# Optimization experiments

Hardware: AMD Instinct MI355X
Metric: run time of the kernel (lower is better)

The kernel has to match this reference:

```python
import jax, jax.numpy as jnp
import numpy as np

K_NEIGHBORS = 16
IGNORE_INDEX = -1
LOSS_WEIGHT = 1.0
N_POINTS = 262144
NUM_CLASSES = 20


def setup_inputs() -> dict:
    key = jax.random.key(0)
    k1, k2, k3, k4 = jax.random.split(key, 4)
    seg_logits = jax.random.normal(k1, (N_POINTS, NUM_CLASSES), dtype=jnp.float32)
    coord = jax.random.normal(k2, (N_POINTS, 3), dtype=jnp.float32)
    labels = jax.random.randint(k3, (N_POINTS,), 0, NUM_CLASSES, dtype=jnp.int64)
    # KNN indices are computed under no_grad in the original (pointops.knn_query);
    # here they are synthetic in-range indices (no -1 padding entries).
    reference_index = jax.random.randint(k4, (N_POINTS, K_NEIGHBORS), 0, N_POINTS, dtype=jnp.int64)
    return {
        "seg_logits": seg_logits,
        "coord": coord,
        "labels": labels,
        "reference_index": reference_index,
    }


def reference(seg_logits, coord, labels, reference_index):
    # coord is only used by the (no-grad) KNN query in the original; indices are given.
    probs = jax.nn.softmax(seg_logits, axis=1)              # [N, C]
    idx = jnp.maximum(reference_index, 0)                   # safe gather index
    knn_mask = reference_index >= 0                         # sign(idx+1).bool()
    neighbor_labels = labels[idx]                           # [N, k]
    same_label_mask = labels[:, None] == neighbor_labels
    center_valid = (labels != IGNORE_INDEX)[:, None]
    neighbor_valid = neighbor_labels != IGNORE_INDEX
    total_mask = knn_mask & center_valid & neighbor_valid & same_label_mask  # [N, k]

    neighbor_probs = probs[idx]                             # [N, k, C]
    prob_dist_sq = jnp.sum((probs[:, None, :] - neighbor_probs) ** 2, axis=2)  # [N, k]
    sum_loss = jnp.sum(prob_dist_sq * total_mask.astype(probs.dtype))
    num_valid = jnp.maximum(jnp.sum(total_mask).astype(probs.dtype), 1.0)
    return (sum_loss / num_valid) * LOSS_WEIGHT
```

## Files before the change

### kernel.cpp

```cpp
#include <hip/hip_runtime.h>

#define NCLS 20
#define IGNORE_INDEX (-1)
#define TPB 128
#define PAIRS_PER_THREAD 8
#define PPB (TPB * PAIRS_PER_THREAD)
#define BLOCKS 4096
#define RBITS 18

__device__ __forceinline__ void softmax_row(const float* __restrict__ row, float* v) {
    const float4* r4 = (const float4*)row;
#pragma unroll
    for (int q = 0; q < 5; ++q) {
        float4 t = r4[q];
        v[4 * q + 0] = t.x; v[4 * q + 1] = t.y;
        v[4 * q + 2] = t.z; v[4 * q + 3] = t.w;
    }
    float mx = v[0];
#pragma unroll
    for (int c = 1; c < NCLS; ++c) mx = fmaxf(mx, v[c]);
    float s = 0.f;
#pragma unroll
    for (int c = 0; c < NCLS; ++c) { v[c] = __expf(v[c] - mx); s += v[c]; }
    float inv = 1.0f / s;
#pragma unroll
    for (int c = 0; c < NCLS; ++c) v[c] *= inv;
}

__global__ __launch_bounds__(TPB) void fused_kernel(
    const float* __restrict__ logits, const int* __restrict__ labels,
    const int* __restrict__ ref_idx,
    unsigned int* __restrict__ counts, float* __restrict__ partials,
    long long total_pairs) {
    __shared__ unsigned int s_buf[PPB];
    __shared__ int s_cnt;
    __shared__ float s_wsum[TPB / 64];
    const int tid = threadIdx.x;
    if (tid == 0) s_cnt = 0;
    __syncthreads();

    const long long pair0 = (long long)blockIdx.x * PPB + (long long)tid * 8;
    if (pair0 + 8 <= total_pairs) {
        const int p = (int)(pair0 >> 4);
        const int li = labels[p];
        int4 ra = *(const int4*)(ref_idx + pair0);
        int4 rb = *(const int4*)(ref_idx + pair0 + 4);
        int rr[8] = {ra.x, ra.y, ra.z, ra.w, rb.x, rb.y, rb.z, rb.w};
        int nl[8];
#pragma unroll
        for (int j = 0; j < 8; ++j) nl[j] = labels[max(rr[j], 0)];
        if (li != IGNORE_INDEX) {
#pragma unroll
            for (int j = 0; j < 8; ++j) {
                if (rr[j] >= 0 && nl[j] == li) {
                    int slot = atomicAdd(&s_cnt, 1);
                    s_buf[slot] = ((unsigned int)(tid * 8 + j) << RBITS) |
                                  (unsigned int)rr[j];
                }
            }
        }
    }
    __syncthreads();
    const int c = s_cnt;

    float fsum = 0.f;
    for (int i = tid; i < c; i += TPB) {
        unsigned int e = s_buf[i];
        unsigned int lid = e >> RBITS;
        unsigned int r = e & ((1u << RBITS) - 1u);
        unsigned int p = (unsigned int)blockIdx.x * (PPB / 16) + (lid >> 4);
        float a[NCLS], b[NCLS];
        softmax_row(logits + (size_t)p * NCLS, a);
        softmax_row(logits + (size_t)r * NCLS, b);
        float d = 0.f;
#pragma unroll
        for (int k = 0; k < NCLS; ++k) {
            float dx = a[k] - b[k];
            d = fmaf(dx, dx, d);
        }
        fsum += d;
    }

#pragma unroll
    for (int off = 32; off > 0; off >>= 1) fsum += __shfl_down(fsum, off, 64);
    if ((tid & 63) == 0) s_wsum[tid >> 6] = fsum;
    __syncthreads();
    if (tid == 0) {
        float t = 0.f;
#pragma unroll
        for (int w = 0; w < TPB / 64; ++w) t += s_wsum[w];
        partials[blockIdx.x] = t;
        counts[blockIdx.x] = (unsigned int)c;
    }
}

__global__ __launch_bounds__(1024) void reduce_kernel(
    const float* __restrict__ partials, const unsigned int* __restrict__ counts,
    float* __restrict__ out, int m) {
    double dsum = 0.0;
    unsigned long long cnt = 0;
    for (int i = threadIdx.x; i < m; i += 1024) {
        dsum += (double)partials[i];
        cnt  += (unsigned long long)min(counts[i], (unsigned int)PPB);
    }
#pragma unroll
    for (int off = 32; off > 0; off >>= 1) {
        dsum += __shfl_down(dsum, off, 64);
        cnt  += __shfl_down(cnt,  off, 64);
    }
    __shared__ double s_sum[16];
    __shared__ unsigned long long s_cnt[16];
    const int wave = threadIdx.x >> 6;
    if ((threadIdx.x & 63) == 0) { s_sum[wave] = dsum; s_cnt[wave] = cnt; }
    __syncthreads();
    if (threadIdx.x == 0) {
        double ts = 0.0; unsigned long long tc = 0;
        for (int w = 0; w < 16; ++w) { ts += s_sum[w]; tc += s_cnt[w]; }
        if (tc < 1ull) tc = 1ull;
        out[0] = (float)(ts / (double)tc);
    }
}

extern "C" void kernel_launch(void* const* d_in, const int* in_sizes, int n_in,
                              void* d_out, int out_size, void* d_ws, size_t ws_size,
                              hipStream_t stream) {
    const float* seg_logits = (const float*)d_in[0];
    const int* labels  = (const int*)d_in[2];
    const int* ref_idx = (const int*)d_in[3];
    float* out = (float*)d_out;
    const int n = in_sizes[2];
    const long long total_pairs = (long long)n * 16;

    unsigned int* counts = (unsigned int*)d_ws;
    float* partials      = (float*)((char*)d_ws + BLOCKS * 4);

    fused_kernel<<<BLOCKS, TPB, 0, stream>>>(seg_logits, labels, ref_idx,
                                             counts, partials, total_pairs);
    reduce_kernel<<<1, 1024, 0, stream>>>(partials, counts, out, BLOCKS);
}
```

Baseline: 103.0 us.

## Cache center softmax rows in LDS and use wave-aggregated compaction atomics

Each block now computes the softmax for its 64 center points once and stores it in shared memory, so the pair loop only recomputes softmax for the neighbor row instead of both rows. The per-pair shared atomicAdd in compaction is replaced by a ballot/popcount scheme with one atomic per wave per neighbor slot. Index loads become nontemporal and the grid size is derived from the input size. This cuts redundant exp and logit loads for centers (about 1 in 20 pairs are kept) at the cost of extra LDS and a center-softmax phase run by half the threads.

```diff
diff --git a/kernel.cpp b/kernel.cpp
--- a/kernel.cpp
+++ b/kernel.cpp
@@ -5,8 +5,11 @@
 #define TPB 128
 #define PAIRS_PER_THREAD 8
 #define PPB (TPB * PAIRS_PER_THREAD)
-#define BLOCKS 4096
+#define CENTERS_PER_BLOCK (PPB / 16)
 #define RBITS 18
+#define PSTRIDE 21
+
+typedef int iv4 __attribute__((ext_vector_type(4)));
 
 __device__ __forceinline__ void softmax_row(const float* __restrict__ row, float* v) {
     const float4* r4 = (const float4*)row;
@@ -33,31 +36,57 @@
     unsigned int* __restrict__ counts, float* __restrict__ partials,
     long long total_pairs) {
     __shared__ unsigned int s_buf[PPB];
+    __shared__ float s_probs[CENTERS_PER_BLOCK][PSTRIDE];
     __shared__ int s_cnt;
     __shared__ float s_wsum[TPB / 64];
-    const int tid = threadIdx.x;
+    const int tid  = threadIdx.x;
+    const int lane = tid & 63;
     if (tid == 0) s_cnt = 0;
     __syncthreads();
 
     const long long pair0 = (long long)blockIdx.x * PPB + (long long)tid * 8;
-    if (pair0 + 8 <= total_pairs) {
+    const bool inb = (pair0 + 8 <= total_pairs);
+    int li = IGNORE_INDEX;
+    int rr[8] = {-1, -1, -1, -1, -1, -1, -1, -1};
+    int nl[8];
+    if (inb) {
         const int p = (int)(pair0 >> 4);
-        const int li = labels[p];
-        int4 ra = *(const int4*)(ref_idx + pair0);
-        int4 rb = *(const int4*)(ref_idx + pair0 + 4);
-        int rr[8] = {ra.x, ra.y, ra.z, ra.w, rb.x, rb.y, rb.z, rb.w};
-        int nl[8];
+        li = labels[p];
+        const iv4* rp = (const iv4*)(ref_idx + pair0);
+        iv4 ra = __builtin_nontemporal_load(rp);
+        iv4 rb = __builtin_nontemporal_load(rp + 1);
+        rr[0] = ra.x; rr[1] = ra.y; rr[2] = ra.z; rr[3] = ra.w;
+        rr[4] = rb.x; rr[5] = rb.y; rr[6] = rb.z; rr[7] = rb.w;
 #pragma unroll
         for (int j = 0; j < 8; ++j) nl[j] = labels[max(rr[j], 0)];
-        if (li != IGNORE_INDEX) {
+    } else {
 #pragma unroll
-            for (int j = 0; j < 8; ++j) {
-                if (rr[j] >= 0 && nl[j] == li) {
-                    int slot = atomicAdd(&s_cnt, 1);
-                    s_buf[slot] = ((unsigned int)(tid * 8 + j) << RBITS) |
-                                  (unsigned int)rr[j];
-                }
-            }
+        for (int j = 0; j < 8; ++j) nl[j] = IGNORE_INDEX - 1;
+    }
+
+    const int p0 = blockIdx.x * CENTERS_PER_BLOCK;
+    if (tid < CENTERS_PER_BLOCK) {
+        float v[NCLS];
+        softmax_row(logits + (size_t)(p0 + tid) * NCLS, v);
+#pragma unroll
+        for (int c2 = 0; c2 < NCLS; ++c2) s_probs[tid][c2] = v[c2];
+    }
+
+    const unsigned long long lt_mask = (1ull << lane) - 1ull;
+#pragma unroll
+    for (int j = 0; j < 8; ++j) {
+        const bool keep = (rr[j] >= 0) && (nl[j] == li) && (li != IGNORE_INDEX);
+        unsigned long long m = __ballot(keep);
+        int base = 0;
+        if (lane == 0) {
+            int tot = __popcll(m);
+            if (tot) base = atomicAdd(&s_cnt, tot);
+        }
+        base = __shfl(base, 0, 64);
+        if (keep) {
+            int pre = __popcll(m & lt_mask);
+            s_buf[base + pre] = ((unsigned int)(tid * 8 + j) << RBITS) |
+                                (unsigned int)rr[j];
         }
     }
     __syncthreads();
@@ -65,17 +94,16 @@
 
     float fsum = 0.f;
     for (int i = tid; i < c; i += TPB) {
-        unsigned int e = s_buf[i];
+        unsigned int e   = s_buf[i];
         unsigned int lid = e >> RBITS;
-        unsigned int r = e & ((1u << RBITS) - 1u);
-        unsigned int p = (unsigned int)blockIdx.x * (PPB / 16) + (lid >> 4);
-        float a[NCLS], b[NCLS];
-        softmax_row(logits + (size_t)p * NCLS, a);
+        unsigned int r   = e & ((1u << RBITS) - 1u);
+        const float* pa  = s_probs[lid >> 4];
+        float b[NCLS];
         softmax_row(logits + (size_t)r * NCLS, b);
         float d = 0.f;
 #pragma unroll
         for (int k = 0; k < NCLS; ++k) {
-            float dx = a[k] - b[k];
+            float dx = pa[k] - b[k];
             d = fmaf(dx, dx, d);
         }
         fsum += d;
@@ -130,11 +158,12 @@
     float* out = (float*)d_out;
     const int n = in_sizes[2];
     const long long total_pairs = (long long)n * 16;
+    const int blocks = (int)((total_pairs + PPB - 1) / PPB);
 
     unsigned int* counts = (unsigned int*)d_ws;
-    float* partials      = (float*)((char*)d_ws + BLOCKS * 4);
+    float* partials      = (float*)((char*)d_ws + (size_t)blocks * 4);
 
-    fused_kernel<<<BLOCKS, TPB, 0, stream>>>(seg_logits, labels, ref_idx,
+    fused_kernel<<<blocks, TPB, 0, stream>>>(seg_logits, labels, ref_idx,
                                              counts, partials, total_pairs);
-    reduce_kernel<<<1, 1024, 0, stream>>>(partials, counts, out, BLOCKS);
+    reduce_kernel<<<1, 1024, 0, stream>>>(partials, counts, out, blocks);
 }
```

Result: slower. 105.4 us (+2.4%).
